# Performance work log

Hardware: AMD Instinct MI355X
Metric: run time of the kernel (lower is better)

The kernel has to match this reference:

```python
import jax, jax.numpy as jnp
import numpy as np

N, E = 50000, 800000
IN_DIM, HEADS, C1, C2, OUT_DIM = 256, 8, 64, 32, 40
NEG_SLOPE = 0.2  # PyG GATConv leaky_relu slope


def setup_inputs() -> dict:
    key = jax.random.key(0)
    ks = jax.random.split(key, 12)
    g = lambda k, shp, fan: jax.random.normal(k, shp, jnp.float32) / np.float32(np.sqrt(fan))
    return {
        "x": jax.random.normal(ks[0], (N, IN_DIM), jnp.float32),
        "edge_index": jax.random.randint(ks[1], (2, E), 0, N, dtype=jnp.int32),
        # layer 1: GATConv(IN_DIM -> C1, heads=HEADS, concat=True)
        "W1": g(ks[2], (IN_DIM, HEADS * C1), IN_DIM),
        "att_src1": g(ks[3], (HEADS, C1), C1),
        "att_dst1": g(ks[4], (HEADS, C1), C1),
        "b1": jnp.zeros((HEADS * C1,), jnp.float32),
        # layer 2: GATConv(HEADS*C1 -> C2, heads=1, concat=False)
        "W2": g(ks[5], (HEADS * C1, C2), HEADS * C1),
        "att_src2": g(ks[6], (1, C2), C2),
        "att_dst2": g(ks[7], (1, C2), C2),
        "b2": jnp.zeros((C2,), jnp.float32),
        # final linear head
        "fcW": g(ks[8], (C2, OUT_DIM), C2),
        "fcb": jnp.zeros((OUT_DIM,), jnp.float32),
    }


def gat_conv(x, src, dst, W, att_src, att_dst, bias, heads, ch, concat):
    """PyG-style GATConv: gather -> per-edge attention -> segment softmax -> scatter."""
    n = x.shape[0]
    xl = (x @ W).reshape(n, heads, ch)                       # [N,H,C]
    a_src = jnp.einsum('nhc,hc->nh', xl, att_src)            # [N,H]
    a_dst = jnp.einsum('nhc,hc->nh', xl, att_dst)
    e = jax.nn.leaky_relu(a_src[src] + a_dst[dst], NEG_SLOPE)  # [E,H]
    emax = jax.ops.segment_max(e, dst, num_segments=n)
    emax = jnp.where(jnp.isfinite(emax), emax, 0.0)
    p = jnp.exp(e - emax[dst])
    denom = jax.ops.segment_sum(p, dst, num_segments=n)
    alpha = p / (denom[dst] + 1e-16)                         # [E,H]
    out = jax.ops.segment_sum(xl[src] * alpha[:, :, None], dst, num_segments=n)  # [N,H,C]
    out = out.reshape(n, heads * ch) if concat else out.mean(axis=1)
    return out + bias


def reference(x, edge_index, W1, att_src1, att_dst1, b1,
              W2, att_src2, att_dst2, b2, fcW, fcb):
    n = x.shape[0]
    loop = jnp.arange(n, dtype=edge_index.dtype)             # add_self_loops (PyG default)
    src = jnp.concatenate([edge_index[0], loop])
    dst = jnp.concatenate([edge_index[1], loop])
    h = jax.nn.relu(gat_conv(x, src, dst, W1, att_src1, att_dst1, b1, HEADS, C1, True))
    h = jax.nn.relu(gat_conv(h, src, dst, W2, att_src2, att_dst2, b2, 1, C2, False))
    embedding = h                                            # [N, C2]
    logits = h @ fcW + fcb                                   # [N, OUT_DIM]
    return (embedding, logits)
```

## Files before the change

### kernel.cpp

```cpp
#include <hip/hip_runtime.h>
#include <hip/hip_bf16.h>
#include <math.h>

#define NEG_SLOPE 0.2f

typedef __attribute__((ext_vector_type(8))) short bf16x8;
typedef __attribute__((ext_vector_type(4))) float f32x4;

__device__ __forceinline__ float lrelu(float x) { return x > 0.f ? x : NEG_SLOPE * x; }
__device__ __forceinline__ float blo(unsigned u) { return __uint_as_float(u << 16); }
__device__ __forceinline__ float bhi(unsigned u) { return __uint_as_float(u & 0xffff0000u); }
__device__ __forceinline__ unsigned short f2b(float f) {
    __hip_bfloat16 b = __float2bfloat16(f);
    return *(unsigned short*)&b;
}
__device__ __forceinline__ int ktrue(int k) {
    int pl = k & 63;
    return (k & ~63) + ((pl & 3) << 4) + (pl >> 2);
}

__global__ __launch_bounds__(256) void prep_kernel(
    const float* __restrict__ W1, unsigned short* __restrict__ W1T,
    const float* __restrict__ W2, unsigned short* __restrict__ W2T,
    const int* __restrict__ ei, int E, int EL, int* __restrict__ deg,
    int b_cw)
{
    const int b = blockIdx.x;
    if (b < b_cw) {
        int i = b * 256 + threadIdx.x;
        if (i < 512 * 256) {
            int nn = i >> 8, k = i & 255;
            W1T[nn * 256 + k] = f2b(W1[k * 512 + nn]);
        } else if (i < 512 * 256 + 32 * 512) {
            int j = i - 512 * 256;
            int c = j >> 9, k = j & 511;
            W2T[c * 512 + k] = f2b(W2[ktrue(k) * 32 + c]);
        }
    } else {
        int base = (b - b_cw) * 1024 + threadIdx.x;
        #pragma unroll
        for (int k = 0; k < 4; ++k) {
            int e = base + k * 256;
            if (e < EL) {
                int d = (e < E) ? ei[E + e] : e - E;
                atomicAdd(&deg[d << 4], 1);
            }
        }
    }
}

__global__ __launch_bounds__(256) void scan1_kernel(
    const int* __restrict__ deg, int* __restrict__ bsum, int n)
{
    __shared__ int red[256];
    int t = threadIdx.x, i = blockIdx.x * 256 + t;
    red[t] = (i < n) ? deg[i << 4] : 0;
    __syncthreads();
    for (int off = 128; off > 0; off >>= 1) {
        if (t < off) red[t] += red[t + off];
        __syncthreads();
    }
    if (t == 0) bsum[blockIdx.x] = red[0];
}

__global__ __launch_bounds__(256) void scan2_kernel(
    const int* __restrict__ bsum, int* __restrict__ bsoff, int B)
{
    __shared__ int part[256];
    int t = threadIdx.x;
    int v = (t < B) ? bsum[t] : 0;
    part[t] = v;
    __syncthreads();
    for (int off = 1; off < 256; off <<= 1) {
        int tmp = (t >= off) ? part[t - off] : 0;
        __syncthreads();
        part[t] += tmp;
        __syncthreads();
    }
    if (t < B) bsoff[t] = part[t] - v;
}

__global__ __launch_bounds__(256) void scan3_kernel(
    const int* __restrict__ deg, const int* __restrict__ bsoff,
    int* __restrict__ rowptr, int* __restrict__ cursor, int n, int EL)
{
    __shared__ int part[256];
    int t = threadIdx.x, b = blockIdx.x, i = b * 256 + t;
    int v = (i < n) ? deg[i << 4] : 0;
    part[t] = v;
    __syncthreads();
    for (int off = 1; off < 256; off <<= 1) {
        int tmp = (t >= off) ? part[t - off] : 0;
        __syncthreads();
        part[t] += tmp;
        __syncthreads();
    }
    if (i < n) {
        int r = bsoff[b] + part[t] - v;
        rowptr[i] = r;
        cursor[i << 4] = r;
    }
    if (i == n - 1) rowptr[n] = EL;
}

__global__ __launch_bounds__(256) void scatter_gemm1_kernel(
    const int* __restrict__ ei, int E, int EL,
    int* __restrict__ cursor, int* __restrict__ csr_src,
    const float* __restrict__ x, const unsigned short* __restrict__ W1T,
    unsigned char* __restrict__ xl1q, float* __restrict__ ascale,
    const float* __restrict__ att_src, const float* __restrict__ att_dst,
    float* __restrict__ a_dst,
    int M, int b_sc)
{
    if (blockIdx.x < b_sc) {
        const int base = blockIdx.x * 1024 + threadIdx.x;
        int s0 = 0, s1 = 0, s2 = 0, s3 = 0;
        int d0 = 0, d1 = 0, d2 = 0, d3 = 0;
        const int e0 = base, e1 = base + 256, e2 = base + 512, e3 = base + 768;
        if (e0 < EL) { if (e0 < E) { s0 = ei[e0]; d0 = ei[E + e0]; } else s0 = d0 = e0 - E; }
        if (e1 < EL) { if (e1 < E) { s1 = ei[e1]; d1 = ei[E + e1]; } else s1 = d1 = e1 - E; }
        if (e2 < EL) { if (e2 < E) { s2 = ei[e2]; d2 = ei[E + e2]; } else s2 = d2 = e2 - E; }
        if (e3 < EL) { if (e3 < E) { s3 = ei[e3]; d3 = ei[E + e3]; } else s3 = d3 = e3 - E; }
        int p0 = 0, p1 = 0, p2 = 0, p3 = 0;
        if (e0 < EL) p0 = atomicAdd(&cursor[d0 << 4], 1);
        if (e1 < EL) p1 = atomicAdd(&cursor[d1 << 4], 1);
        if (e2 < EL) p2 = atomicAdd(&cursor[d2 << 4], 1);
        if (e3 < EL) p3 = atomicAdd(&cursor[d3 << 4], 1);
        if (e0 < EL) csr_src[p0] = s0;
        if (e1 < EL) csr_src[p1] = s1;
        if (e2 < EL) csr_src[p2] = s2;
        if (e3 < EL) csr_src[p3] = s3;
        return;
    }
    __shared__ unsigned short As[128 * 40];
    __shared__ unsigned short Bs[128 * 40];
    const int tt  = blockIdx.x - b_sc;
    const int nt4 = gridDim.x - b_sc;
    int tr, tc;
    if (tt < (nt4 & ~31)) { tr = ((tt >> 5) << 3) + (tt & 7); tc = (tt >> 3) & 3; }
    else                  { tr = tt >> 2;                      tc = tt & 3; }
    const int row0 = tr * 128;
    const int col0 = tc * 128;
    const int tid  = threadIdx.x;
    const int wave = tid >> 6;
    const int wrow = wave >> 1;
    const int wcol = wave & 1;
    const int lane = tid & 63;
    const int quad = lane >> 4;
    const int l15  = lane & 15;
    const int sm = tid >> 1;
    const int sk = (tid & 1) * 16;

    f32x4 acc[4][4] = {};

    for (int kb = 0; kb < 256; kb += 32) {
        uint4 a0 = make_uint4(0, 0, 0, 0), a1 = make_uint4(0, 0, 0, 0);
        if (row0 + sm < M) {
            const float4* ap = (const float4*)(x + (size_t)(row0 + sm) * 256 + kb + sk);
            float4 f0 = ap[0], f1 = ap[1], f2 = ap[2], f3 = ap[3];
            a0.x = (unsigned)f2b(f0.x) | ((unsigned)f2b(f0.y) << 16);
            a0.y = (unsigned)f2b(f0.z) | ((unsigned)f2b(f0.w) << 16);
            a0.z = (unsigned)f2b(f1.x) | ((unsigned)f2b(f1.y) << 16);
            a0.w = (unsigned)f2b(f1.z) | ((unsigned)f2b(f1.w) << 16);
            a1.x = (unsigned)f2b(f2.x) | ((unsigned)f2b(f2.y) << 16);
            a1.y = (unsigned)f2b(f2.z) | ((unsigned)f2b(f2.w) << 16);
            a1.z = (unsigned)f2b(f3.x) | ((unsigned)f2b(f3.y) << 16);
            a1.w = (unsigned)f2b(f3.z) | ((unsigned)f2b(f3.w) << 16);
        }
        uint4* adp = (uint4*)&As[sm * 40 + sk];
        adp[0] = a0; adp[1] = a1;
        const uint4* bp = (const uint4*)(W1T + (size_t)(col0 + sm) * 256 + kb + sk);
        uint4* bd = (uint4*)&Bs[sm * 40 + sk];
        bd[0] = bp[0]; bd[1] = bp[1];
        __syncthreads();
        bf16x8 af[4], bf[4];
        #pragma unroll
        for (int mf = 0; mf < 4; ++mf)
            af[mf] = *(const bf16x8*)&As[(wrow * 64 + mf * 16 + l15) * 40 + quad * 8];
        #pragma unroll
        for (int nf = 0; nf < 4; ++nf)
            bf[nf] = *(const bf16x8*)&Bs[(wcol * 64 + nf * 16 + l15) * 40 + quad * 8];
        #pragma unroll
        for (int mf = 0; mf < 4; ++mf)
            #pragma unroll
            for (int nf = 0; nf < 4; ++nf)
                acc[mf][nf] = __builtin_amdgcn_mfma_f32_16x16x32_bf16(
                    af[mf], bf[nf], acc[mf][nf], 0, 0, 0);
        __syncthreads();
    }

    const int h = tc * 2 + wcol;
    float asv[4], adv[4];
    #pragma unroll
    for (int nf = 0; nf < 4; ++nf) {
        asv[nf] = att_src[h * 64 + nf * 16 + l15];
        adv[nf] = att_dst[h * 64 + nf * 16 + l15];
    }
    #pragma unroll
    for (int mf = 0; mf < 4; ++mf) {
        #pragma unroll
        for (int r = 0; r < 4; ++r) {
            const int row = row0 + wrow * 64 + mf * 16 + quad * 4 + r;
            float v0 = acc[mf][0][r], v1 = acc[mf][1][r];
            float v2 = acc[mf][2][r], v3 = acc[mf][3][r];
            float sv = v0 * asv[0] + v1 * asv[1] + v2 * asv[2] + v3 * asv[3];
            float tv = v0 * adv[0] + v1 * adv[1] + v2 * adv[2] + v3 * adv[3];
            sv += __shfl_xor(sv, 1); tv += __shfl_xor(tv, 1);
            sv += __shfl_xor(sv, 2); tv += __shfl_xor(tv, 2);
            sv += __shfl_xor(sv, 4); tv += __shfl_xor(tv, 4);
            sv += __shfl_xor(sv, 8); tv += __shfl_xor(tv, 8);
            float m4 = fmaxf(fmaxf(fabsf(v0), fabsf(v1)), fmaxf(fabsf(v2), fabsf(v3)));
            m4 = fmaxf(m4, __shfl_xor(m4, 1));
            m4 = fmaxf(m4, __shfl_xor(m4, 2));
            m4 = fmaxf(m4, __shfl_xor(m4, 4));
            m4 = fmaxf(m4, __shfl_xor(m4, 8));
            const float invs = (m4 > 0.f) ? 127.f / m4 : 0.f;
            int q0 = __float2int_rn(v0 * invs); q0 = max(-127, min(127, q0));
            int q1 = __float2int_rn(v1 * invs); q1 = max(-127, min(127, q1));
            int q2 = __float2int_rn(v2 * invs); q2 = max(-127, min(127, q2));
            int q3 = __float2int_rn(v3 * invs); q3 = max(-127, min(127, q3));
            unsigned pkq = (unsigned)(q0 + 128) | ((unsigned)(q1 + 128) << 8) |
                           ((unsigned)(q2 + 128) << 16) | ((unsigned)(q3 + 128) << 24);
            if (row < M) {
                *(unsigned*)(xl1q + (size_t)row * 512 + h * 64 + l15 * 4) = pkq;
                if (l15 == 0) {
                    *(float2*)(ascale + (size_t)row * 16 + h * 2) =
                        make_float2(sv, m4 * (1.f / 127.f));
                    a_dst[row * 8 + h] = tv;
                }
            }
        }
    }
}

__global__ __launch_bounds__(256) void gather1_kernel(
    const int* __restrict__ rowptr, const int* __restrict__ csr_src,
    const unsigned char* __restrict__ xl1q, const float* __restrict__ ascale,
    const float* __restrict__ a_dst, const float* __restrict__ b1,
    unsigned short* __restrict__ h1, int M)
{
    int wid  = (blockIdx.x * blockDim.x + threadIdx.x) >> 6;
    int lane = threadIdx.x & 63;
    if (wid >= M) return;
    const int start = rowptr[wid], end = rowptr[wid + 1];
    const int h0 = lane >> 3;
    const float adh = a_dst[wid * 8 + h0];
    float dsum = 0.f, csum = 0.f;
    float acc0 = 0.f, acc1 = 0.f, acc2 = 0.f, acc3 = 0.f;
    float acc4 = 0.f, acc5 = 0.f, acc6 = 0.f, acc7 = 0.f;

#define G1_LOAD(AS, V, idx) do {                                              \
        if ((idx) < end) {                                                    \
            int s_ = csr_src[idx];                                            \
            AS = *(const float2*)(ascale + (size_t)s_ * 16 + h0 * 2);         \
            V  = *(const uint2*)(xl1q + (size_t)s_ * 512 + (lane << 3));      \
        } else { AS = make_float2(-1e30f, 0.f); V = make_uint2(0u, 0u); }     \
    } while (0)

#define G1_CONS(AS, V) do {                                                   \
        float p_ = __expf(lrelu((AS).x + adh));                               \
        dsum += p_;                                                           \
        float sa_ = p_ * (AS).y;                                              \
        csum += sa_;                                                          \
        acc0 += (float)( (V).x        & 0xffu) * sa_;                         \
        acc1 += (float)(((V).x >>  8) & 0xffu) * sa_;                         \
        acc2 += (float)(((V).x >> 16) & 0xffu) * sa_;                         \
        acc3 += (float)( (V).x >> 24         ) * sa_;                         \
        acc4 += (float)( (V).y        & 0xffu) * sa_;                         \
        acc5 += (float)(((V).y >>  8) & 0xffu) * sa_;                         \
        acc6 += (float)(((V).y >> 16) & 0xffu) * sa_;                         \
        acc7 += (float)( (V).y >> 24         ) * sa_;                         \
    } while (0)

    float2 as0, as1, as2, as3;
    uint2  v0, v1, v2, v3;
    G1_LOAD(as0, v0, start);
    G1_LOAD(as1, v1, start + 1);
    G1_LOAD(as2, v2, start + 2);
    G1_LOAD(as3, v3, start + 3);
    for (int j = start; j < end; j += 4) {
        float2 na0, na1, na2, na3;
        uint2  nv0, nv1, nv2, nv3;
        G1_LOAD(na0, nv0, j + 4);
        G1_LOAD(na1, nv1, j + 5);
        G1_LOAD(na2, nv2, j + 6);
        G1_LOAD(na3, nv3, j + 7);
        G1_CONS(as0, v0);
        G1_CONS(as1, v1);
        G1_CONS(as2, v2);
        G1_CONS(as3, v3);
        as0 = na0; v0 = nv0; as1 = na1; v1 = nv1;
        as2 = na2; v2 = nv2; as3 = na3; v3 = nv3;
    }
#undef G1_LOAD
#undef G1_CONS

    const float inv = 1.f / (dsum + 1e-16f);
    const float c128 = 128.f * csum;
    const int pg = lane << 3;
    float bj[8];
    #pragma unroll
    for (int j = 0; j < 8; ++j) {
        int pl = (pg + j) & 63;
        bj[j] = b1[(pg & ~63) + ((pl & 3) << 4) + (pl >> 2)];
    }
    float o0 = fmaxf((acc0 - c128) * inv + bj[0], 0.f);
    float o1 = fmaxf((acc1 - c128) * inv + bj[1], 0.f);
    float o2 = fmaxf((acc2 - c128) * inv + bj[2], 0.f);
    float o3 = fmaxf((acc3 - c128) * inv + bj[3], 0.f);
    float o4 = fmaxf((acc4 - c128) * inv + bj[4], 0.f);
    float o5 = fmaxf((acc5 - c128) * inv + bj[5], 0.f);
    float o6 = fmaxf((acc6 - c128) * inv + bj[6], 0.f);
    float o7 = fmaxf((acc7 - c128) * inv + bj[7], 0.f);
    uint4 pk;
    pk.x = (unsigned)f2b(o0) | ((unsigned)f2b(o1) << 16);
    pk.y = (unsigned)f2b(o2) | ((unsigned)f2b(o3) << 16);
    pk.z = (unsigned)f2b(o4) | ((unsigned)f2b(o5) << 16);
    pk.w = (unsigned)f2b(o6) | ((unsigned)f2b(o7) << 16);
    ((uint4*)(h1 + (size_t)wid * 512))[lane] = pk;
}

__global__ __launch_bounds__(256) void gemm2_mfma_kernel(
    const unsigned short* __restrict__ h1, const unsigned short* __restrict__ W2T,
    const float* __restrict__ att_src2, const float* __restrict__ att_dst2,
    unsigned short* __restrict__ xl2b, float* __restrict__ a_src2, float* __restrict__ a_dst2,
    int M)
{
    __shared__ unsigned short As[128 * 72];
    __shared__ unsigned short Bs[32 * 72];
    const int tid  = threadIdx.x;
    const int row0 = blockIdx.x * 128;
    const int wv   = tid >> 6;
    const int lane = tid & 63;
    const int quad = lane >> 4;
    const int l15  = lane & 15;

    f32x4 acc[2][2] = {};

    for (int kb = 0; kb < 512; kb += 64) {
        #pragma unroll
        for (int i = 0; i < 4; ++i) {
            int u = tid + 256 * i;
            int r = u >> 3;
            int kq = (u & 7) * 8;
            uint4 v = make_uint4(0, 0, 0, 0);
            if (row0 + r < M)
                v = *(const uint4*)(h1 + (size_t)(row0 + r) * 512 + kb + kq);
            *(uint4*)&As[r * 72 + kq] = v;
        }
        {
            int r = tid >> 3;
            int kq = (tid & 7) * 8;
            *(uint4*)&Bs[r * 72 + kq] = *(const uint4*)(W2T + (size_t)r * 512 + kb + kq);
        }
        __syncthreads();

        #pragma unroll
        for (int ks = 0; ks < 2; ++ks) {
            bf16x8 af[2], bf[2];
            #pragma unroll
            for (int mf = 0; mf < 2; ++mf)
                af[mf] = *(const bf16x8*)&As[(wv * 32 + mf * 16 + l15) * 72 + ks * 32 + quad * 8];
            #pragma unroll
            for (int nf = 0; nf < 2; ++nf)
                bf[nf] = *(const bf16x8*)&Bs[(nf * 16 + l15) * 72 + ks * 32 + quad * 8];
            #pragma unroll
            for (int mf = 0; mf < 2; ++mf)
                #pragma unroll
                for (int nf = 0; nf < 2; ++nf)
                    acc[mf][nf] = __builtin_amdgcn_mfma_f32_16x16x32_bf16(
                        af[mf], bf[nf], acc[mf][nf], 0, 0, 0);
        }
        __syncthreads();
    }

    float as2v[2], ad2v[2];
    #pragma unroll
    for (int nf = 0; nf < 2; ++nf) {
        as2v[nf] = att_src2[nf * 16 + l15];
        ad2v[nf] = att_dst2[nf * 16 + l15];
    }
    #pragma unroll
    for (int mf = 0; mf < 2; ++mf) {
        #pragma unroll
        for (int r = 0; r < 4; ++r) {
            const int row = row0 + wv * 32 + mf * 16 + quad * 4 + r;
            float v0 = acc[mf][0][r], v1 = acc[mf][1][r];
            float sv = v0 * as2v[0] + v1 * as2v[1];
            float tv = v0 * ad2v[0] + v1 * ad2v[1];
            sv += __shfl_xor(sv, 1); tv += __shfl_xor(tv, 1);
            sv += __shfl_xor(sv, 2); tv += __shfl_xor(tv, 2);
            sv += __shfl_xor(sv, 4); tv += __shfl_xor(tv, 4);
            sv += __shfl_xor(sv, 8); tv += __shfl_xor(tv, 8);
            if (row < M) {
                xl2b[(size_t)row * 32 + l15]      = f2b(v0);
                xl2b[(size_t)row * 32 + 16 + l15] = f2b(v1);
                if (l15 == 0) { a_src2[row] = sv; a_dst2[row] = tv; }
            }
        }
    }
}

__global__ __launch_bounds__(256) void gather2_head_kernel(
    const int* __restrict__ rowptr, const int* __restrict__ csr_src,
    const unsigned short* __restrict__ xl2b, const float* __restrict__ a_src2,
    const float* __restrict__ a_dst2, const float* __restrict__ b2,
    const float* __restrict__ fcW, const float* __restrict__ fcb,
    float* __restrict__ emb, float* __restrict__ logits, int M)
{
    __shared__ float sw[32][40];
    for (int i = threadIdx.x; i < 32 * 40; i += 256) sw[i / 40][i % 40] = fcW[i];
    __syncthreads();
    int wid  = (blockIdx.x * blockDim.x + threadIdx.x) >> 6;
    int lane = threadIdx.x & 63;
    if (wid >= M) return;
    const int start = rowptr[wid], end = rowptr[wid + 1];
    const float ad = a_dst2[wid];
    const int g  = lane >> 4;
    const int c2 = lane & 15;

#define G2_LOAD(A, U, idx) do {                                               \
        if ((idx) < end) {                                                    \
            int s_ = csr_src[idx];                                            \
            A = a_src2[s_];                                                   \
            U = *(const unsigned*)(xl2b + (size_t)s_ * 32 + 2 * c2);          \
        } else { A = -1e30f; U = 0u; }                                        \
    } while (0)

    float dsum = 0.f;
    float accx = 0.f, accy = 0.f;
    float a0, a1;
    unsigned u0, u1;
    G2_LOAD(a0, u0, start + g);
    G2_LOAD(a1, u1, start + g + 4);
    for (int j = start + g; j < end; j += 8) {
        float na0, na1;
        unsigned nu0, nu1;
        G2_LOAD(na0, nu0, j + 8);
        G2_LOAD(na1, nu1, j + 12);
        {
            float p = __expf(lrelu(a0 + ad));
            dsum += p;
            accx += p * blo(u0);
            accy += p * bhi(u0);
        }
        {
            float p = __expf(lrelu(a1 + ad));
            dsum += p;
            accx += p * blo(u1);
            accy += p * bhi(u1);
        }
        a0 = na0; u0 = nu0; a1 = na1; u1 = nu1;
    }
#undef G2_LOAD
    dsum += __shfl_xor(dsum, 16); accx += __shfl_xor(accx, 16); accy += __shfl_xor(accy, 16);
    dsum += __shfl_xor(dsum, 32); accx += __shfl_xor(accx, 32); accy += __shfl_xor(accy, 32);
    const float inv = 1.f / (dsum + 1e-16f);
    const float2 b2v = *(const float2*)(b2 + 2 * c2);
    float ex = fmaxf(accx * inv + b2v.x, 0.f);
    float ey = fmaxf(accy * inv + b2v.y, 0.f);
    if (g == 0) *(float2*)(emb + (size_t)wid * 32 + 2 * c2) = make_float2(ex, ey);
    const int col = (lane < 40) ? lane : 0;
    float lsum = (lane < 40) ? fcb[col] : 0.f;
    #pragma unroll
    for (int k = 0; k < 16; ++k) {
        float vx = __shfl(ex, k);
        float vy = __shfl(ey, k);
        lsum += vx * sw[2 * k][col] + vy * sw[2 * k + 1][col];
    }
    if (lane < 40) logits[(size_t)wid * 40 + lane] = lsum;
}

extern "C" void kernel_launch(void* const* d_in, const int* in_sizes, int n_in,
                              void* d_out, int out_size, void* d_ws, size_t ws_size,
                              hipStream_t stream)
{
    const float* x   = (const float*)d_in[0];
    const int*   ei  = (const int*)d_in[1];
    const float* W1  = (const float*)d_in[2];
    const float* as1 = (const float*)d_in[3];
    const float* ad1 = (const float*)d_in[4];
    const float* b1  = (const float*)d_in[5];
    const float* W2  = (const float*)d_in[6];
    const float* as2 = (const float*)d_in[7];
    const float* ad2 = (const float*)d_in[8];
    const float* b2  = (const float*)d_in[9];
    const float* fcW = (const float*)d_in[10];
    const float* fcb = (const float*)d_in[11];

    const int n  = in_sizes[0] / 256;
    const int e  = in_sizes[1] / 2;
    const int el = e + n;

    char* ws = (char*)d_ws;
    size_t off = 0;
    unsigned short* w1t  = (unsigned short*)(ws + off); off += (size_t)512 * 256 * 2;
    unsigned short* w2t  = (unsigned short*)(ws + off); off += (size_t)32 * 512 * 2;
    unsigned char*  xl1q = (unsigned char*)(ws + off);  off += (size_t)n * 512;
    float* ascale = (float*)(ws + off); off += (size_t)n * 16 * 4;
    unsigned short* h1   = (unsigned short*)(ws + off); off += (size_t)n * 512 * 2;
    unsigned short* xl2b = (unsigned short*)(ws + off); off += (size_t)n * 32 * 2;
    float* a_dst1 = (float*)(ws + off); off += (size_t)n * 8 * 4;
    float* a_src2 = (float*)(ws + off); off += (size_t)n * 4;
    float* a_dst2 = (float*)(ws + off); off += (size_t)n * 4;
    int*   deg    = (int*)(ws + off);   off += (size_t)n * 16 * 4;
    int*   cursor = (int*)(ws + off);   off += (size_t)n * 16 * 4;
    int*   rowptr = (int*)(ws + off);   off += (size_t)(n + 1) * 4;
    int*   csr_src= (int*)(ws + off);   off += (size_t)el * 4;
    int*   bsum   = (int*)(ws + off);   off += 256 * 4;
    int*   bsoff  = (int*)(ws + off);   off += 256 * 4;

    float* emb    = (float*)d_out;
    float* logits = (float*)d_out + (size_t)n * 32;

    hipMemsetAsync(deg, 0, (size_t)n * 16 * 4, stream);

    const int b_cw = (512 * 256 + 32 * 512 + 255) / 256;
    const int b_dg = (el + 1023) / 1024;
    prep_kernel<<<b_cw + b_dg, 256, 0, stream>>>(
        W1, w1t, W2, w2t, ei, e, el, deg, b_cw);

    const int nb = (n + 255) / 256;
    scan1_kernel<<<nb, 256, 0, stream>>>(deg, bsum, n);
    scan2_kernel<<<1, 256, 0, stream>>>(bsum, bsoff, nb);
    scan3_kernel<<<nb, 256, 0, stream>>>(deg, bsoff, rowptr, cursor, n, el);

    const int b_sc = (el + 1023) / 1024;
    const int n_tiles_y = (n + 127) / 128;
    scatter_gemm1_kernel<<<b_sc + 4 * n_tiles_y, 256, 0, stream>>>(
        ei, e, el, cursor, csr_src,
        x, w1t, xl1q, ascale, as1, ad1, a_dst1, n, b_sc);

    gather1_kernel<<<((size_t)n * 64 + 255) / 256, 256, 0, stream>>>(
        rowptr, csr_src, xl1q, ascale, a_dst1, b1, h1, n);
    gemm2_mfma_kernel<<<(n + 127) / 128, 256, 0, stream>>>(
        h1, w2t, as2, ad2, xl2b, a_src2, a_dst2, n);
    gather2_head_kernel<<<((size_t)n * 64 + 255) / 256, 256, 0, stream>>>(
        rowptr, csr_src, xl2b, a_src2, a_dst2, b2, fcW, fcb, emb, logits, n);
}
```

Measured before the change: 391.2 us.

## Bucket edges by destination range before CSR scatter for atomic locality

The degree-count pass now also partitions edges into 8 buckets by destination-node range, staging (src,dst) pairs in the h1 workspace, with an overflow list for full buckets. The CSR scatter blocks then each process one bucket, so the cursor atomics and csr_src writes of a block group touch a narrower address range and stay more cache-local. The cost is an extra write and read of the edge pairs, shared-memory atomics in prep, and a fixed scatter block count of 832.

After: 402.4 us. +2.9%, slower.

```diff
diff --git a/kernel.cpp b/kernel.cpp
--- a/kernel.cpp
+++ b/kernel.cpp
@@ -3,6 +3,7 @@
 #include <math.h>
 
 #define NEG_SLOPE 0.2f
+#define PCAP 131072
 
 typedef __attribute__((ext_vector_type(8))) short bf16x8;
 typedef __attribute__((ext_vector_type(4))) float f32x4;
@@ -19,11 +20,14 @@
     return (k & ~63) + ((pl & 3) << 4) + (pl >> 2);
 }
 
+
 __global__ __launch_bounds__(256) void prep_kernel(
     const float* __restrict__ W1, unsigned short* __restrict__ W1T,
     const float* __restrict__ W2, unsigned short* __restrict__ W2T,
     const int* __restrict__ ei, int E, int EL, int* __restrict__ deg,
-    int b_cw)
+    int* __restrict__ pfill, int* __restrict__ ofill,
+    uint2* __restrict__ pedges, uint2* __restrict__ oedges,
+    int PN, int b_cw)
 {
     const int b = blockIdx.x;
     if (b < b_cw) {
@@ -36,17 +40,47 @@
             int c = j >> 9, k = j & 511;
             W2T[c * 512 + k] = f2b(W2[ktrue(k) * 32 + c]);
         }
-    } else {
-        int base = (b - b_cw) * 1024 + threadIdx.x;
-        #pragma unroll
-        for (int k = 0; k < 4; ++k) {
-            int e = base + k * 256;
-            if (e < EL) {
-                int d = (e < E) ? ei[E + e] : e - E;
-                atomicAdd(&deg[d << 4], 1);
-            }
-        }
-    }
+        return;
+    }
+    __shared__ int lcnt[8];
+    __shared__ int lbase[8];
+    const int tid = threadIdx.x;
+    const int base = (b - b_cw) * 1024 + tid;
+    const int e0 = base, e1 = base + 256, e2 = base + 512, e3 = base + 768;
+    const bool v0 = e0 < EL, v1 = e1 < EL, v2 = e2 < EL, v3 = e3 < EL;
+    int s0 = 0, s1 = 0, s2 = 0, s3 = 0;
+    int d0 = 0, d1 = 0, d2 = 0, d3 = 0;
+    if (v0) { if (e0 < E) { s0 = ei[e0]; d0 = ei[E + e0]; } else s0 = d0 = e0 - E; }
+    if (v1) { if (e1 < E) { s1 = ei[e1]; d1 = ei[E + e1]; } else s1 = d1 = e1 - E; }
+    if (v2) { if (e2 < E) { s2 = ei[e2]; d2 = ei[E + e2]; } else s2 = d2 = e2 - E; }
+    if (v3) { if (e3 < E) { s3 = ei[e3]; d3 = ei[E + e3]; } else s3 = d3 = e3 - E; }
+    if (v0) atomicAdd(&deg[d0 << 4], 1);
+    if (v1) atomicAdd(&deg[d1 << 4], 1);
+    if (v2) atomicAdd(&deg[d2 << 4], 1);
+    if (v3) atomicAdd(&deg[d3 << 4], 1);
+    if (tid < 8) lcnt[tid] = 0;
+    __syncthreads();
+    int q0 = 0, q1 = 0, q2 = 0, q3 = 0;
+    int r0 = 0, r1 = 0, r2 = 0, r3 = 0;
+    if (v0) { q0 = d0 / PN; r0 = atomicAdd(&lcnt[q0], 1); }
+    if (v1) { q1 = d1 / PN; r1 = atomicAdd(&lcnt[q1], 1); }
+    if (v2) { q2 = d2 / PN; r2 = atomicAdd(&lcnt[q2], 1); }
+    if (v3) { q3 = d3 / PN; r3 = atomicAdd(&lcnt[q3], 1); }
+    __syncthreads();
+    if (tid < 8) lbase[tid] = atomicAdd(&pfill[tid << 4], lcnt[tid]);
+    __syncthreads();
+    if (v0) { int sl = lbase[q0] + r0;
+        if (sl < PCAP) pedges[(size_t)q0 * PCAP + sl] = make_uint2((unsigned)s0, (unsigned)d0);
+        else { int os = atomicAdd(&ofill[0], 1); oedges[os] = make_uint2((unsigned)s0, (unsigned)d0); } }
+    if (v1) { int sl = lbase[q1] + r1;
+        if (sl < PCAP) pedges[(size_t)q1 * PCAP + sl] = make_uint2((unsigned)s1, (unsigned)d1);
+        else { int os = atomicAdd(&ofill[0], 1); oedges[os] = make_uint2((unsigned)s1, (unsigned)d1); } }
+    if (v2) { int sl = lbase[q2] + r2;
+        if (sl < PCAP) pedges[(size_t)q2 * PCAP + sl] = make_uint2((unsigned)s2, (unsigned)d2);
+        else { int os = atomicAdd(&ofill[0], 1); oedges[os] = make_uint2((unsigned)s2, (unsigned)d2); } }
+    if (v3) { int sl = lbase[q3] + r3;
+        if (sl < PCAP) pedges[(size_t)q3 * PCAP + sl] = make_uint2((unsigned)s3, (unsigned)d3);
+        else { int os = atomicAdd(&ofill[0], 1); oedges[os] = make_uint2((unsigned)s3, (unsigned)d3); } }
 }
 
 __global__ __launch_bounds__(256) void scan1_kernel(
@@ -104,7 +138,8 @@
 }
 
 __global__ __launch_bounds__(256) void scatter_gemm1_kernel(
-    const int* __restrict__ ei, int E, int EL,
+    const uint2* __restrict__ pedges, const uint2* __restrict__ oedges,
+    const int* __restrict__ pfill, const int* __restrict__ ofill,
     int* __restrict__ cursor, int* __restrict__ csr_src,
     const float* __restrict__ x, const unsigned short* __restrict__ W1T,
     unsigned char* __restrict__ xl1q, float* __restrict__ ascale,
@@ -113,23 +148,36 @@
     int M, int b_sc)
 {
     if (blockIdx.x < b_sc) {
-        const int base = blockIdx.x * 1024 + threadIdx.x;
-        int s0 = 0, s1 = 0, s2 = 0, s3 = 0;
-        int d0 = 0, d1 = 0, d2 = 0, d3 = 0;
-        const int e0 = base, e1 = base + 256, e2 = base + 512, e3 = base + 768;
-        if (e0 < EL) { if (e0 < E) { s0 = ei[e0]; d0 = ei[E + e0]; } else s0 = d0 = e0 - E; }
-        if (e1 < EL) { if (e1 < E) { s1 = ei[e1]; d1 = ei[E + e1]; } else s1 = d1 = e1 - E; }
-        if (e2 < EL) { if (e2 < E) { s2 = ei[e2]; d2 = ei[E + e2]; } else s2 = d2 = e2 - E; }
-        if (e3 < EL) { if (e3 < E) { s3 = ei[e3]; d3 = ei[E + e3]; } else s3 = d3 = e3 - E; }
-        int p0 = 0, p1 = 0, p2 = 0, p3 = 0;
-        if (e0 < EL) p0 = atomicAdd(&cursor[d0 << 4], 1);
-        if (e1 < EL) p1 = atomicAdd(&cursor[d1 << 4], 1);
-        if (e2 < EL) p2 = atomicAdd(&cursor[d2 << 4], 1);
-        if (e3 < EL) p3 = atomicAdd(&cursor[d3 << 4], 1);
-        if (e0 < EL) csr_src[p0] = s0;
-        if (e1 < EL) csr_src[p1] = s1;
-        if (e2 < EL) csr_src[p2] = s2;
-        if (e3 < EL) csr_src[p3] = s3;
+        const int tid = threadIdx.x;
+        const int p   = blockIdx.x & 7;
+        const int bi  = blockIdx.x >> 3;
+        const int str = (b_sc >> 3) * 256;
+        int cnt = pfill[p << 4]; if (cnt > PCAP) cnt = PCAP;
+        const uint2* pe = pedges + (size_t)p * PCAP;
+        for (int i0 = bi * 256 + tid; i0 < cnt; i0 += 4 * str) {
+            const int i1 = i0 + str, i2 = i0 + 2 * str, i3 = i0 + 3 * str;
+            const bool w1 = i1 < cnt, w2 = i2 < cnt, w3 = i3 < cnt;
+            uint2 ed0 = pe[i0];
+            uint2 ed1 = w1 ? pe[i1] : ed0;
+            uint2 ed2 = w2 ? pe[i2] : ed0;
+            uint2 ed3 = w3 ? pe[i3] : ed0;
+            int p0 = atomicAdd(&cursor[ed0.y << 4], 1);
+            int p1 = w1 ? atomicAdd(&cursor[ed1.y << 4], 1) : 0;
+            int p2 = w2 ? atomicAdd(&cursor[ed2.y << 4], 1) : 0;
+            int p3 = w3 ? atomicAdd(&cursor[ed3.y << 4], 1) : 0;
+            csr_src[p0] = ed0.x;
+            if (w1) csr_src[p1] = ed1.x;
+            if (w2) csr_src[p2] = ed2.x;
+            if (w3) csr_src[p3] = ed3.x;
+        }
+        if (p == 0) {
+            int oc = ofill[0];
+            for (int i = bi * 256 + tid; i < oc; i += str) {
+                uint2 ed = oedges[i];
+                int pos = atomicAdd(&cursor[ed.y << 4], 1);
+                csr_src[pos] = ed.x;
+            }
+        }
         return;
     }
     __shared__ unsigned short As[128 * 40];
@@ -491,6 +539,7 @@
     const int n  = in_sizes[0] / 256;
     const int e  = in_sizes[1] / 2;
     const int el = e + n;
+    const int pn = (((n + 7) / 8) + 63) & ~63;
 
     char* ws = (char*)d_ws;
     size_t off = 0;
@@ -504,31 +553,36 @@
     float* a_src2 = (float*)(ws + off); off += (size_t)n * 4;
     float* a_dst2 = (float*)(ws + off); off += (size_t)n * 4;
     int*   deg    = (int*)(ws + off);   off += (size_t)n * 16 * 4;
+    int*   pfill  = (int*)(ws + off);   off += 8 * 16 * 4;
+    int*   ofill  = (int*)(ws + off);   off += 16 * 4;
     int*   cursor = (int*)(ws + off);   off += (size_t)n * 16 * 4;
     int*   rowptr = (int*)(ws + off);   off += (size_t)(n + 1) * 4;
     int*   csr_src= (int*)(ws + off);   off += (size_t)el * 4;
     int*   bsum   = (int*)(ws + off);   off += 256 * 4;
     int*   bsoff  = (int*)(ws + off);   off += 256 * 4;
 
+    uint2* pedges = (uint2*)h1;
+    uint2* oedges = (uint2*)h1 + (size_t)8 * PCAP;
+
     float* emb    = (float*)d_out;
     float* logits = (float*)d_out + (size_t)n * 32;
 
-    hipMemsetAsync(deg, 0, (size_t)n * 16 * 4, stream);
+    hipMemsetAsync(deg, 0, ((size_t)n * 16 + 8 * 16 + 16) * 4, stream);
 
     const int b_cw = (512 * 256 + 32 * 512 + 255) / 256;
     const int b_dg = (el + 1023) / 1024;
     prep_kernel<<<b_cw + b_dg, 256, 0, stream>>>(
-        W1, w1t, W2, w2t, ei, e, el, deg, b_cw);
+        W1, w1t, W2, w2t, ei, e, el, deg, pfill, ofill, pedges, oedges, pn, b_cw);
 
     const int nb = (n + 255) / 256;
     scan1_kernel<<<nb, 256, 0, stream>>>(deg, bsum, n);
     scan2_kernel<<<1, 256, 0, stream>>>(bsum, bsoff, nb);
     scan3_kernel<<<nb, 256, 0, stream>>>(deg, bsoff, rowptr, cursor, n, el);
 
-    const int b_sc = (el + 1023) / 1024;
+    const int b_sc = 832;
     const int n_tiles_y = (n + 127) / 128;
     scatter_gemm1_kernel<<<b_sc + 4 * n_tiles_y, 256, 0, stream>>>(
-        ei, e, el, cursor, csr_src,
+        pedges, oedges, pfill, ofill, cursor, csr_src,
         x, w1t, xl1q, ascale, as1, ad1, a_dst1, n, b_sc);
 
     gather1_kernel<<<((size_t)n * 64 + 255) / 256, 256, 0, stream>>>(
```
